# Performance work log

Measured on AMD Instinct MI355X. Metric: run time of the kernel, lower is better.

## Reference

```python
import jax, jax.numpy as jnp
import numpy as np
import math

B, N0, DEG = 32, 1584, 4
E = B * N0 * DEG
FIN, HID, EDIM, ROUTE, HEADS = 32, 64, 8, 16, 4
NEG = 0.2  # leaky_relu negative slope (alpha)
K1 = math.ceil(0.8 * N0)   # 1268 nodes/graph after pool1
K2 = math.ceil(0.8 * K1)   # 1015 after pool2
K3 = math.ceil(0.8 * K2)   # 812 after pool3


def _gatv2(x, src, dst, emask, edge_attr, Wl, bl, Wr, br, We, att, bo, num_nodes):
    # PyG GATv2Conv, concat=False (mean over heads), edge_dim, eval mode (no dropout)
    xl = (x @ Wl + bl).reshape(-1, HEADS, HID)            # source transform  [N,H,C]
    xr = (x @ Wr + br).reshape(-1, HEADS, HID)            # target transform  [N,H,C]
    ee = (edge_attr @ We).reshape(-1, HEADS, HID)         # edge transform    [E,H,C]
    m = jax.nn.leaky_relu(xl[src] + xr[dst] + ee, NEG)    # [E,H,C]
    logits = jnp.einsum('ehc,hc->eh', m, att)             # [E,H]
    logits = jnp.where(emask[:, None], logits, -jnp.inf)
    mx = jax.ops.segment_max(logits, dst, num_segments=num_nodes)
    mx = jnp.where(jnp.isfinite(mx), mx, 0.0)             # nodes w/o in-edges
    ex = jnp.where(emask[:, None], jnp.exp(logits - mx[dst]), 0.0)
    den = jax.ops.segment_sum(ex, dst, num_segments=num_nodes)
    alpha = ex / jnp.maximum(den[dst], 1e-16)             # segment softmax over dst
    out = jax.ops.segment_sum(alpha[:, :, None] * xl[src], dst, num_segments=num_nodes)
    return out.mean(axis=1) + bo                          # concat=False -> head mean


def _topk(x, src, dst, emask, w, n_per, k):
    # PyG TopKPooling(ratio=0.8): score = tanh(x.w/||w||); keep top-k per graph,
    # scale kept features by score; keep edges whose endpoints both survive.
    s = jnp.tanh((x @ w) / jnp.linalg.norm(w))            # [B*n_per]
    _, idx = jax.lax.top_k(s.reshape(B, n_per), k)        # [B,k]
    perm = (idx + jnp.arange(B)[:, None] * n_per).reshape(-1)
    x_new = x[perm] * s[perm][:, None]
    new_id = jnp.full((B * n_per,), -1, jnp.int32).at[perm].set(
        jnp.arange(B * k, dtype=jnp.int32))
    nsrc, ndst = new_id[src], new_id[dst]
    m = emask & (nsrc >= 0) & (ndst >= 0)
    return x_new, jnp.where(m, nsrc, 0), jnp.where(m, ndst, 0), m


def _readout(x, k):
    # global mean pool || global max pool (nodes are grouped per graph, k each)
    xb = x.reshape(B, k, HID)
    return jnp.concatenate([xb.mean(1), xb.max(1)], axis=1)


def _forward(x, edge_attr, edge_index,
             g1_Wl, g1_bl, g1_Wr, g1_br, g1_We, g1_att, g1_b,
             g2_Wl, g2_bl, g2_Wr, g2_br, g2_We, g2_att, g2_b,
             g3_Wl, g3_bl, g3_Wr, g3_br, g3_We, g3_att, g3_b,
             p1_w, p2_w, p3_w,
             fc1_W, fc1_b, fc2_W, fc2_b, fc3_W, fc3_b):
    src, dst = edge_index[0], edge_index[1]
    emask = jnp.ones((E,), bool)
    h = jax.nn.relu(_gatv2(x, src, dst, emask, edge_attr,
                           g1_Wl, g1_bl, g1_Wr, g1_br, g1_We, g1_att, g1_b, B * N0))
    h, src, dst, emask = _topk(h, src, dst, emask, p1_w, N0, K1)
    x1 = _readout(h, K1)
    h = jax.nn.relu(_gatv2(h, src, dst, emask, edge_attr,
                           g2_Wl, g2_bl, g2_Wr, g2_br, g2_We, g2_att, g2_b, B * K1))
    h, src, dst, emask = _topk(h, src, dst, emask, p2_w, K1, K2)
    x2 = _readout(h, K2)
    h = jax.nn.relu(_gatv2(h, src, dst, emask, edge_attr,
                           g3_Wl, g3_bl, g3_Wr, g3_br, g3_We, g3_att, g3_b, B * K2))
    h, src, dst, emask = _topk(h, src, dst, emask, p3_w, K2, K3)
    x3 = _readout(h, K3)
    r = x1 + x2 + x3                                      # [B, 2*HID]
    h = jax.nn.relu(r @ fc1_W + fc1_b)
    h = jax.nn.relu(h @ fc2_W + fc2_b)                    # dropout results unused in source
    return jax.nn.softmax(h @ fc3_W + fc3_b, axis=1)      # [B, ROUTE]


def setup_inputs() -> dict:
    key = jax.random.key(0)
    ks = iter(jax.random.split(key, 64))
    def nrm(shape, scale):
        return jax.random.normal(next(ks), shape, jnp.float32) * scale
    x = nrm((B * N0, FIN), 1.0)
    srcl = jax.random.randint(next(ks), (B, N0 * DEG), 0, N0)
    dstl = jax.random.randint(next(ks), (B, N0 * DEG), 0, N0)
    off = (jnp.arange(B) * N0)[:, None]
    edge_index = jnp.stack([(srcl + off).reshape(-1),
                            (dstl + off).reshape(-1)]).astype(jnp.int32)
    edge_attr = nrm((E, EDIM), 1.0)
    batch = jnp.repeat(jnp.arange(B, dtype=jnp.int32), N0)
    inp = {"x": x, "edge_attr": edge_attr, "edge_index": edge_index, "batch": batch}
    for li, fin in ((1, FIN), (2, HID), (3, HID)):
        g = 1.0 / np.sqrt(fin)
        inp[f"g{li}_Wl"] = nrm((fin, HEADS * HID), g)
        inp[f"g{li}_bl"] = nrm((HEADS * HID,), 0.02)
        inp[f"g{li}_Wr"] = nrm((fin, HEADS * HID), g)
        inp[f"g{li}_br"] = nrm((HEADS * HID,), 0.02)
        inp[f"g{li}_We"] = nrm((EDIM, HEADS * HID), 1.0 / np.sqrt(EDIM))
        inp[f"g{li}_att"] = nrm((HEADS, HID), 1.0 / np.sqrt(HID))
        inp[f"g{li}_b"] = nrm((HID,), 0.02)
    for li in (1, 2, 3):
        inp[f"p{li}_w"] = nrm((HID,), 1.0 / np.sqrt(HID))
    for fin, fout, nm in ((2 * HID, HID, "fc1"), (HID, HID, "fc2"), (HID, ROUTE, "fc3")):
        inp[f"{nm}_W"] = nrm((fin, fout), 1.0 / np.sqrt(fin))
        inp[f"{nm}_b"] = nrm((fout,), 0.02)
    return inp


def reference(x, edge_attr, edge_index, batch,
              g1_Wl, g1_bl, g1_Wr, g1_br, g1_We, g1_att, g1_b,
              g2_Wl, g2_bl, g2_Wr, g2_br, g2_We, g2_att, g2_b,
              g3_Wl, g3_bl, g3_Wr, g3_br, g3_We, g3_att, g3_b,
              p1_w, p2_w, p3_w,
              fc1_W, fc1_b, fc2_W, fc2_b, fc3_W, fc3_b):
    # batch is implicit: nodes are laid out grouped per graph with static sizes
    del batch
    return _forward(x, edge_attr, edge_index,
                    g1_Wl, g1_bl, g1_Wr, g1_br, g1_We, g1_att, g1_b,
                    g2_Wl, g2_bl, g2_Wr, g2_br, g2_We, g2_att, g2_b,
                    g3_Wl, g3_bl, g3_Wr, g3_br, g3_We, g3_att, g3_b,
                    p1_w, p2_w, p3_w,
                    fc1_W, fc1_b, fc2_W, fc2_b, fc3_W, fc3_b)
```

## Files before the change

kernel.cpp:

```cpp
#include <hip/hip_runtime.h>

typedef unsigned short u16;
typedef unsigned int u32;
typedef unsigned long long u64;

#define E_TOT 202752
#define NMAX  50688
#define HEADS 4
#define B_    32
#define MAXDEG 32

#define CDIV(a,b) (((a)+(b)-1)/(b))

__device__ __forceinline__ u32 ford(float f) {
  u32 u = __float_as_uint(f);
  return (u & 0x80000000u) ? ~u : (u | 0x80000000u);
}
__device__ __forceinline__ float ford_inv(u32 u) {
  u32 b = (u & 0x80000000u) ? (u ^ 0x80000000u) : ~u;
  return __uint_as_float(b);
}

__global__ void k_edge_init_csr(const int* __restrict__ ei, int* __restrict__ src,
                                int* __restrict__ dst, int* __restrict__ em,
                                int* __restrict__ cnt, int* __restrict__ csr) {
  int e = blockIdx.x * blockDim.x + threadIdx.x;
  if (e >= E_TOT) return;
  int s = ei[e], d = ei[E_TOT + e];
  src[e] = s;
  dst[e] = d;
  em[e] = 1;
  int pos = atomicAdd(&cnt[d], 1);
  if (pos < MAXDEG) csr[d * MAXDEG + pos] = e;
}

template <int FIN>
__global__ void k_transform_t(const float* __restrict__ hin,
                              const float* __restrict__ Wl, const float* __restrict__ bl,
                              const float* __restrict__ Wr, const float* __restrict__ br,
                              float* __restrict__ xl, float* __restrict__ xr) {
  __shared__ float xs[8][FIN];
  int n0 = blockIdx.x * 8, j = threadIdx.x;
  for (int t = j; t < 8 * FIN; t += 256)
    xs[t >> (FIN == 32 ? 5 : 6)][t & (FIN - 1)] =
        hin[(size_t)(n0 + (t >> (FIN == 32 ? 5 : 6))) * FIN + (t & (FIN - 1))];
  __syncthreads();
  float al[8], ar[8];
  float blv = bl[j], brv = br[j];
#pragma unroll
  for (int t = 0; t < 8; ++t) { al[t] = blv; ar[t] = brv; }
  for (int i = 0; i < FIN; ++i) {
    float wl = Wl[i * 256 + j], wr = Wr[i * 256 + j];
#pragma unroll
    for (int t = 0; t < 8; ++t) {
      float xv = xs[t][i];
      al[t] += xv * wl;
      ar[t] += xv * wr;
    }
  }
#pragma unroll
  for (int t = 0; t < 8; ++t) {
    xl[(size_t)(n0 + t) * 256 + j] = al[t];
    xr[(size_t)(n0 + t) * 256 + j] = ar[t];
  }
}

__global__ void k_gat_fused(const int* __restrict__ srcv, const int* __restrict__ cnt,
                            const int* __restrict__ csr, const float* __restrict__ ea,
                            const float* __restrict__ We, const float* __restrict__ att,
                            const float* __restrict__ xl, const float* __restrict__ xr,
                            const float* __restrict__ bias, const float* __restrict__ pwv,
                            float* __restrict__ out, float* __restrict__ sc, int N) {
  int n = blockIdx.x * 4 + (threadIdx.x >> 6);
  int lane = threadIdx.x & 63;
  int cg = lane & 15;
  int cb = (lane >> 4) * 64 + cg * 4;
  if (n >= N) return;
  int deg = min(cnt[n], MAXDEG);
  int e_l = 0, s_l = 0;
  if (lane < deg) { e_l = csr[n * MAXDEG + lane]; s_l = srcv[e_l]; }
  float4 xd4 = *(const float4*)(xr + (size_t)n * 256 + cb);
  float4 at4 = *(const float4*)(att + cb);
  float4 w0 = *(const float4*)(We + 0 * 256 + cb);
  float4 w1 = *(const float4*)(We + 1 * 256 + cb);
  float4 w2 = *(const float4*)(We + 2 * 256 + cb);
  float4 w3 = *(const float4*)(We + 3 * 256 + cb);
  float4 w4_ = *(const float4*)(We + 4 * 256 + cb);
  float4 w5 = *(const float4*)(We + 5 * 256 + cb);
  float4 w6 = *(const float4*)(We + 6 * 256 + cb);
  float4 w7 = *(const float4*)(We + 7 * 256 + cb);
  float m = -INFINITY, l = 0.f;
  float ox = 0.f, oy = 0.f, oz = 0.f, ow = 0.f;
  for (int i0 = 0; i0 < deg; i0 += 4) {
    int c0 = deg - i0; if (c0 > 4) c0 = 4;
    float4 xs[4], a0[4], a1[4];
#pragma unroll
    for (int j = 0; j < 4; ++j) {
      int idx = (j < c0) ? (i0 + j) : i0;
      int e = __shfl(e_l, idx, 64);
      int s = __shfl(s_l, idx, 64);
      xs[j] = *(const float4*)(xl + (size_t)s * 256 + cb);
      a0[j] = *(const float4*)(ea + (size_t)e * 8);
      a1[j] = *(const float4*)(ea + (size_t)e * 8 + 4);
    }
#pragma unroll
    for (int j = 0; j < 4; ++j) {
      if (j < c0) {
        float e0 = a0[j].x * w0.x + a0[j].y * w1.x + a0[j].z * w2.x + a0[j].w * w3.x
                 + a1[j].x * w4_.x + a1[j].y * w5.x + a1[j].z * w6.x + a1[j].w * w7.x;
        float e1 = a0[j].x * w0.y + a0[j].y * w1.y + a0[j].z * w2.y + a0[j].w * w3.y
                 + a1[j].x * w4_.y + a1[j].y * w5.y + a1[j].z * w6.y + a1[j].w * w7.y;
        float e2 = a0[j].x * w0.z + a0[j].y * w1.z + a0[j].z * w2.z + a0[j].w * w3.z
                 + a1[j].x * w4_.z + a1[j].y * w5.z + a1[j].z * w6.z + a1[j].w * w7.z;
        float e3 = a0[j].x * w0.w + a0[j].y * w1.w + a0[j].z * w2.w + a0[j].w * w3.w
                 + a1[j].x * w4_.w + a1[j].y * w5.w + a1[j].z * w6.w + a1[j].w * w7.w;
        float m0 = xs[j].x + xd4.x + e0; m0 = (m0 >= 0.f) ? m0 : 0.2f * m0;
        float m1 = xs[j].y + xd4.y + e1; m1 = (m1 >= 0.f) ? m1 : 0.2f * m1;
        float m2 = xs[j].z + xd4.z + e2; m2 = (m2 >= 0.f) ? m2 : 0.2f * m2;
        float m3 = xs[j].w + xd4.w + e3; m3 = (m3 >= 0.f) ? m3 : 0.2f * m3;
        float v = at4.x * m0 + at4.y * m1 + at4.z * m2 + at4.w * m3;
        v += __shfl_xor(v, 1, 64);
        v += __shfl_xor(v, 2, 64);
        v += __shfl_xor(v, 4, 64);
        v += __shfl_xor(v, 8, 64);
        float nm = fmaxf(m, v);
        float scale = __expf(m - nm);
        float p = __expf(v - nm);
        ox = ox * scale + p * xs[j].x;
        oy = oy * scale + p * xs[j].y;
        oz = oz * scale + p * xs[j].z;
        ow = ow * scale + p * xs[j].w;
        l = l * scale + p;
        m = nm;
      }
    }
  }
  float inv = 0.25f / fmaxf(l, 1e-16f);
  float r0 = ox * inv, r1 = oy * inv, r2 = oz * inv, r3 = ow * inv;
  r0 += __shfl_xor(r0, 16, 64); r0 += __shfl_xor(r0, 32, 64);
  r1 += __shfl_xor(r1, 16, 64); r1 += __shfl_xor(r1, 32, 64);
  r2 += __shfl_xor(r2, 16, 64); r2 += __shfl_xor(r2, 32, 64);
  r3 += __shfl_xor(r3, 16, 64); r3 += __shfl_xor(r3, 32, 64);
  float4 bi4 = *(const float4*)(bias + cg * 4);
  r0 = fmaxf(r0 + bi4.x, 0.f); r1 = fmaxf(r1 + bi4.y, 0.f);
  r2 = fmaxf(r2 + bi4.z, 0.f); r3 = fmaxf(r3 + bi4.w, 0.f);
  if (lane < 16) *(float4*)(out + (size_t)n * 64 + cg * 4) = float4{r0, r1, r2, r3};
  float4 pw4 = *(const float4*)(pwv + cg * 4);
  float dot = r0 * pw4.x + r1 * pw4.y + r2 * pw4.z + r3 * pw4.w;
  float wn = pw4.x * pw4.x + pw4.y * pw4.y + pw4.z * pw4.z + pw4.w * pw4.w;
  dot += __shfl_xor(dot, 1, 64); wn += __shfl_xor(wn, 1, 64);
  dot += __shfl_xor(dot, 2, 64); wn += __shfl_xor(wn, 2, 64);
  dot += __shfl_xor(dot, 4, 64); wn += __shfl_xor(wn, 4, 64);
  dot += __shfl_xor(dot, 8, 64); wn += __shfl_xor(wn, 8, 64);
  if (lane == 0) sc[n] = tanhf(dot / sqrtf(wn));
}

__global__ __launch_bounds__(1024) void k_topk(const float* __restrict__ s, int n_per,
                                               int k, int npad,
                                               int* __restrict__ perm, int* __restrict__ new_id) {
  __shared__ u64 kv[2048];
  int b = blockIdx.x, tid = threadIdx.x;
  int base = b * n_per;
  for (int i = tid; i < n_per; i += 1024) new_id[base + i] = -1;
  for (int i = tid; i < npad; i += 1024) {
    u32 sk = (i < n_per) ? ford(s[base + i]) : 0u;
    kv[i] = ((u64)sk << 32) | (u32)(0xFFFFFFFFu - (u32)i);
  }
  __syncthreads();
  for (int kk = 2; kk <= npad; kk <<= 1) {
    for (int j = kk >> 1; j > 0; j >>= 1) {
      for (int i = tid; i < npad; i += 1024) {
        int ixj = i ^ j;
        if (ixj > i) {
          u64 a = kv[i], c = kv[ixj];
          bool after = a < c;
          bool doswap = ((i & kk) == 0) ? after : !after;
          if (doswap) { kv[i] = c; kv[ixj] = a; }
        }
      }
      __syncthreads();
    }
  }
  for (int r = tid; r < k; r += 1024) {
    int old = (int)(0xFFFFFFFFu - (u32)(kv[r] & 0xFFFFFFFFu));
    perm[b * k + r] = base + old;
    new_id[base + old] = b * k + r;
  }
}

__global__ void k_gather(const float* __restrict__ hin, const float* __restrict__ s,
                         const int* __restrict__ perm, float* __restrict__ hout, int n64) {
  int t = blockIdx.x * blockDim.x + threadIdx.x;
  if (t >= n64) return;
  int i = t >> 6, c = t & 63;
  int g = perm[i];
  hout[t] = hin[(size_t)g * 64 + c] * s[g];
}

__global__ void k_remap_csr(int* __restrict__ src, int* __restrict__ dst,
                            int* __restrict__ em, const int* __restrict__ new_id,
                            int* __restrict__ cnt, int* __restrict__ csr) {
  int e = blockIdx.x * blockDim.x + threadIdx.x;
  if (e >= E_TOT) return;
  int ns = new_id[src[e]], nd = new_id[dst[e]];
  int m = em[e] && ns >= 0 && nd >= 0;
  src[e] = m ? ns : 0;
  dst[e] = m ? nd : 0;
  em[e] = m;
  if (m) {
    int pos = atomicAdd(&cnt[nd], 1);
    if (pos < MAXDEG) csr[nd * MAXDEG + pos] = e;
  }
}

__global__ void k_readout_part(const float* __restrict__ h, int k,
                               float* __restrict__ rsum, u32* __restrict__ rmaxI) {
  __shared__ float ps[256], pm[256];
  int b = blockIdx.x, ch = blockIdx.y, t = threadIdx.x;
  int c = t & 63, rg = t >> 6;
  int rpc = (k + 15) >> 4;
  int start = ch * rpc, end = min(k, start + rpc);
  const float* hb = h + (size_t)b * k * 64;
  float sum = 0.f, mx = -INFINITY;
  for (int i = start + rg; i < end; i += 4) {
    float v = hb[(size_t)i * 64 + c];
    sum += v;
    mx = fmaxf(mx, v);
  }
  ps[t] = sum; pm[t] = mx;
  __syncthreads();
  if (t < 64) {
    float s4 = ps[t] + ps[t + 64] + ps[t + 128] + ps[t + 192];
    float m4 = fmaxf(fmaxf(pm[t], pm[t + 64]), fmaxf(pm[t + 128], pm[t + 192]));
    atomicAdd(&rsum[b * 64 + t], s4);
    atomicMax(&rmaxI[b * 64 + t], ford(m4));
  }
}

__global__ void k_readout_fin(const float* __restrict__ rsum, const u32* __restrict__ rmaxI,
                              int k, float* __restrict__ r) {
  int b = blockIdx.x, c = threadIdx.x;
  if (c < 64) r[b * 128 + c] += rsum[b * 64 + c] / (float)k;
  else        r[b * 128 + c] += ford_inv(rmaxI[b * 64 + (c - 64)]);
}

__global__ void k_mlp(const float* __restrict__ r,
                      const float* __restrict__ W1, const float* __restrict__ b1,
                      const float* __restrict__ W2, const float* __restrict__ b2,
                      const float* __restrict__ W3, const float* __restrict__ b3,
                      float* __restrict__ out) {
  __shared__ float v0[128], v1[64], v2[64], lgts[16];
  int b = blockIdx.x, t = threadIdx.x;
  v0[t] = r[b * 128 + t];
  v0[64 + t] = r[b * 128 + 64 + t];
  __syncthreads();
  float a = b1[t];
  for (int i = 0; i < 128; ++i) a += v0[i] * W1[i * 64 + t];
  v1[t] = fmaxf(a, 0.f);
  __syncthreads();
  a = b2[t];
  for (int i = 0; i < 64; ++i) a += v1[i] * W2[i * 64 + t];
  v2[t] = fmaxf(a, 0.f);
  __syncthreads();
  if (t < 16) {
    a = b3[t];
    for (int i = 0; i < 64; ++i) a += v2[i] * W3[i * 16 + t];
    lgts[t] = a;
  }
  __syncthreads();
  if (t == 0) {
    float m = lgts[0];
    for (int j = 1; j < 16; ++j) m = fmaxf(m, lgts[j]);
    float ex[16], sum = 0.f;
    for (int j = 0; j < 16; ++j) { ex[j] = expf(lgts[j] - m); sum += ex[j]; }
    for (int j = 0; j < 16; ++j) out[b * 16 + j] = ex[j] / sum;
  }
}

extern "C" void kernel_launch(void* const* d_in, const int* in_sizes, int n_in,
                              void* d_out, int out_size, void* d_ws, size_t ws_size,
                              hipStream_t stream) {
  (void)in_sizes; (void)n_in; (void)out_size; (void)ws_size;
  const float* x  = (const float*)d_in[0];
  const float* ea = (const float*)d_in[1];
  const int*   ei = (const int*)d_in[2];

  const float *gWl[3], *gbl[3], *gWr[3], *gbr[3], *gWe[3], *gatt[3], *gb[3], *pw[3];
  for (int l = 0; l < 3; ++l) {
    int p0 = 4 + 7 * l;
    gWl[l]  = (const float*)d_in[p0 + 0];
    gbl[l]  = (const float*)d_in[p0 + 1];
    gWr[l]  = (const float*)d_in[p0 + 2];
    gbr[l]  = (const float*)d_in[p0 + 3];
    gWe[l]  = (const float*)d_in[p0 + 4];
    gatt[l] = (const float*)d_in[p0 + 5];
    gb[l]   = (const float*)d_in[p0 + 6];
    pw[l]   = (const float*)d_in[25 + l];
  }
  const float* fc1W = (const float*)d_in[28];
  const float* fc1b = (const float*)d_in[29];
  const float* fc2W = (const float*)d_in[30];
  const float* fc2b = (const float*)d_in[31];
  const float* fc3W = (const float*)d_in[32];
  const float* fc3b = (const float*)d_in[33];

  char* w = (char*)d_ws;
  size_t off = 0;
  auto alloc = [&](size_t bytes) -> void* {
    void* p = w + off;
    off += (bytes + 255) & ~(size_t)255;
    return p;
  };
  float* hbuf = (float*)alloc((size_t)B_ * 1268 * 64 * 4);
  float* xl   = (float*)alloc((size_t)NMAX * 256 * 4);
  float* xr   = (float*)alloc((size_t)NMAX * 256 * 4);
  float* nacc = (float*)alloc((size_t)NMAX * 64 * 4);
  int*   cnt  = (int*)alloc((size_t)NMAX * 4);
  char*  rblk = (char*)alloc(32 * 128 * 4);
  float* rsum = (float*)rblk;
  u32*   rmaxI= (u32*)(rblk + 32 * 64 * 4);
  int*   csr  = (int*)alloc((size_t)NMAX * MAXDEG * 4);
  float* sbuf = (float*)alloc((size_t)NMAX * 4);
  float* rbuf = (float*)alloc(32 * 128 * 4);
  int* src    = (int*)alloc((size_t)E_TOT * 4);
  int* dst    = (int*)alloc((size_t)E_TOT * 4);
  int* em     = (int*)alloc((size_t)E_TOT * 4);
  int* new_id = (int*)alloc((size_t)NMAX * 4);
  int* perm   = (int*)alloc((size_t)32 * 1268 * 4);

  hipMemsetAsync(cnt, 0, (size_t)NMAX * 4, stream);
  k_edge_init_csr<<<CDIV(E_TOT, 256), 256, 0, stream>>>(ei, src, dst, em, cnt, csr);
  hipMemsetAsync(rbuf, 0, 32 * 128 * 4, stream);

  const int Ns[3]    = {50688, 40576, 32480};
  const int npers[3] = {1584, 1268, 1015};
  const int ks[3]    = {1268, 1015, 812};
  const int npads[3] = {2048, 2048, 1024};

  for (int l = 0; l < 3; ++l) {
    int N = Ns[l];
    const float* hin = (l == 0) ? x : hbuf;
    hipMemsetAsync(rblk, 0, 32 * 128 * 4, stream);
    if (l == 0)
      k_transform_t<32><<<N / 8, 256, 0, stream>>>(hin, gWl[l], gbl[l], gWr[l], gbr[l], xl, xr);
    else
      k_transform_t<64><<<N / 8, 256, 0, stream>>>(hin, gWl[l], gbl[l], gWr[l], gbr[l], xl, xr);
    k_gat_fused<<<N / 4, 256, 0, stream>>>(src, cnt, csr, ea, gWe[l], gatt[l],
                                           xl, xr, gb[l], pw[l], nacc, sbuf, N);
    k_topk<<<32, 1024, 0, stream>>>(sbuf, npers[l], ks[l], npads[l], perm, new_id);
    k_gather<<<CDIV(B_ * ks[l] * 64, 256), 256, 0, stream>>>(nacc, sbuf, perm, hbuf,
                                                             B_ * ks[l] * 64);
    if (l < 2) {
      hipMemsetAsync(cnt, 0, (size_t)NMAX * 4, stream);
      k_remap_csr<<<CDIV(E_TOT, 256), 256, 0, stream>>>(src, dst, em, new_id, cnt, csr);
    }
    k_readout_part<<<dim3(32, 16), 256, 0, stream>>>(hbuf, ks[l], rsum, rmaxI);
    k_readout_fin<<<32, 128, 0, stream>>>(rsum, rmaxI, ks[l], rbuf);
  }
  k_mlp<<<32, 64, 0, stream>>>(rbuf, fc1W, fc1b, fc2W, fc2b, fc3W, fc3b, (float*)d_out);
}
```

Baseline: 562.4 us.

## Remap GAT blocks so each graph stays on one XCD and batch softmax updates

The fused GAT kernel now maps block indices so all blocks of a given graph land on the same XCD, given round-robin dispatch of blocks across the 8 XCDs. This keeps the xl/xr gathers for that graph in one XCD's L2 instead of spreading them over all of them. The edge loop is also restructured so four edges' logits are computed and reduced together, followed by one online-softmax rescale per group of four instead of per edge. A launch_bounds hint is added as well. The XCD mapping depends on the dispatch order and adds index arithmetic, and padding each graph to a multiple of 4 nodes adds a few idle waves.

```diff
diff --git a/kernel.cpp b/kernel.cpp
--- a/kernel.cpp
+++ b/kernel.cpp
@@ -65,17 +65,23 @@
   }
 }
 
-__global__ void k_gat_fused(const int* __restrict__ srcv, const int* __restrict__ cnt,
-                            const int* __restrict__ csr, const float* __restrict__ ea,
-                            const float* __restrict__ We, const float* __restrict__ att,
-                            const float* __restrict__ xl, const float* __restrict__ xr,
-                            const float* __restrict__ bias, const float* __restrict__ pwv,
-                            float* __restrict__ out, float* __restrict__ sc, int N) {
-  int n = blockIdx.x * 4 + (threadIdx.x >> 6);
+__global__ __launch_bounds__(256, 4)
+void k_gat_fused(const int* __restrict__ srcv, const int* __restrict__ cnt,
+                 const int* __restrict__ csr, const float* __restrict__ ea,
+                 const float* __restrict__ We, const float* __restrict__ att,
+                 const float* __restrict__ xl, const float* __restrict__ xr,
+                 const float* __restrict__ bias, const float* __restrict__ pwv,
+                 float* __restrict__ out, float* __restrict__ sc,
+                 int nper, int NB) {
+  int b = blockIdx.x;
+  int xcd = b & 7, slot = b >> 3;
+  int g = xcd + 8 * (slot / NB);
+  int ln = (slot % NB) * 4 + (threadIdx.x >> 6);
+  if (ln >= nper) return;
+  int n = g * nper + ln;
   int lane = threadIdx.x & 63;
   int cg = lane & 15;
   int cb = (lane >> 4) * 64 + cg * 4;
-  if (n >= N) return;
   int deg = min(cnt[n], MAXDEG);
   int e_l = 0, s_l = 0;
   if (lane < deg) { e_l = csr[n * MAXDEG + lane]; s_l = srcv[e_l]; }
@@ -93,47 +99,53 @@
   float ox = 0.f, oy = 0.f, oz = 0.f, ow = 0.f;
   for (int i0 = 0; i0 < deg; i0 += 4) {
     int c0 = deg - i0; if (c0 > 4) c0 = 4;
-    float4 xs[4], a0[4], a1[4];
+    float4 xs[4];
+    float v[4];
 #pragma unroll
     for (int j = 0; j < 4; ++j) {
       int idx = (j < c0) ? (i0 + j) : i0;
       int e = __shfl(e_l, idx, 64);
       int s = __shfl(s_l, idx, 64);
       xs[j] = *(const float4*)(xl + (size_t)s * 256 + cb);
-      a0[j] = *(const float4*)(ea + (size_t)e * 8);
-      a1[j] = *(const float4*)(ea + (size_t)e * 8 + 4);
-    }
-#pragma unroll
-    for (int j = 0; j < 4; ++j) {
-      if (j < c0) {
-        float e0 = a0[j].x * w0.x + a0[j].y * w1.x + a0[j].z * w2.x + a0[j].w * w3.x
-                 + a1[j].x * w4_.x + a1[j].y * w5.x + a1[j].z * w6.x + a1[j].w * w7.x;
-        float e1 = a0[j].x * w0.y + a0[j].y * w1.y + a0[j].z * w2.y + a0[j].w * w3.y
-                 + a1[j].x * w4_.y + a1[j].y * w5.y + a1[j].z * w6.y + a1[j].w * w7.y;
-        float e2 = a0[j].x * w0.z + a0[j].y * w1.z + a0[j].z * w2.z + a0[j].w * w3.z
-                 + a1[j].x * w4_.z + a1[j].y * w5.z + a1[j].z * w6.z + a1[j].w * w7.z;
-        float e3 = a0[j].x * w0.w + a0[j].y * w1.w + a0[j].z * w2.w + a0[j].w * w3.w
-                 + a1[j].x * w4_.w + a1[j].y * w5.w + a1[j].z * w6.w + a1[j].w * w7.w;
-        float m0 = xs[j].x + xd4.x + e0; m0 = (m0 >= 0.f) ? m0 : 0.2f * m0;
-        float m1 = xs[j].y + xd4.y + e1; m1 = (m1 >= 0.f) ? m1 : 0.2f * m1;
-        float m2 = xs[j].z + xd4.z + e2; m2 = (m2 >= 0.f) ? m2 : 0.2f * m2;
-        float m3 = xs[j].w + xd4.w + e3; m3 = (m3 >= 0.f) ? m3 : 0.2f * m3;
-        float v = at4.x * m0 + at4.y * m1 + at4.z * m2 + at4.w * m3;
-        v += __shfl_xor(v, 1, 64);
-        v += __shfl_xor(v, 2, 64);
-        v += __shfl_xor(v, 4, 64);
-        v += __shfl_xor(v, 8, 64);
-        float nm = fmaxf(m, v);
-        float scale = __expf(m - nm);
-        float p = __expf(v - nm);
-        ox = ox * scale + p * xs[j].x;
-        oy = oy * scale + p * xs[j].y;
-        oz = oz * scale + p * xs[j].z;
-        ow = ow * scale + p * xs[j].w;
-        l = l * scale + p;
-        m = nm;
-      }
-    }
+      float4 q0 = *(const float4*)(ea + (size_t)e * 8);
+      float4 q1 = *(const float4*)(ea + (size_t)e * 8 + 4);
+      float e0 = q0.x * w0.x + q0.y * w1.x + q0.z * w2.x + q0.w * w3.x
+               + q1.x * w4_.x + q1.y * w5.x + q1.z * w6.x + q1.w * w7.x;
+      float e1 = q0.x * w0.y + q0.y * w1.y + q0.z * w2.y + q0.w * w3.y
+               + q1.x * w4_.y + q1.y * w5.y + q1.z * w6.y + q1.w * w7.y;
+      float e2 = q0.x * w0.z + q0.y * w1.z + q0.z * w2.z + q0.w * w3.z
+               + q1.x * w4_.z + q1.y * w5.z + q1.z * w6.z + q1.w * w7.z;
+      float e3 = q0.x * w0.w + q0.y * w1.w + q0.z * w2.w + q0.w * w3.w
+               + q1.x * w4_.w + q1.y * w5.w + q1.z * w6.w + q1.w * w7.w;
+      float m0 = xs[j].x + xd4.x + e0; m0 = (m0 >= 0.f) ? m0 : 0.2f * m0;
+      float m1 = xs[j].y + xd4.y + e1; m1 = (m1 >= 0.f) ? m1 : 0.2f * m1;
+      float m2 = xs[j].z + xd4.z + e2; m2 = (m2 >= 0.f) ? m2 : 0.2f * m2;
+      float m3 = xs[j].w + xd4.w + e3; m3 = (m3 >= 0.f) ? m3 : 0.2f * m3;
+      v[j] = at4.x * m0 + at4.y * m1 + at4.z * m2 + at4.w * m3;
+    }
+#pragma unroll
+    for (int st = 1; st <= 8; st <<= 1) {
+      v[0] += __shfl_xor(v[0], st, 64);
+      v[1] += __shfl_xor(v[1], st, 64);
+      v[2] += __shfl_xor(v[2], st, 64);
+      v[3] += __shfl_xor(v[3], st, 64);
+    }
+    float vmax = v[0];
+    if (c0 > 1) vmax = fmaxf(vmax, v[1]);
+    if (c0 > 2) vmax = fmaxf(vmax, v[2]);
+    if (c0 > 3) vmax = fmaxf(vmax, v[3]);
+    float nm = fmaxf(m, vmax);
+    float scale = __expf(m - nm);
+    float p0 = __expf(v[0] - nm);
+    float p1 = (c0 > 1) ? __expf(v[1] - nm) : 0.f;
+    float p2 = (c0 > 2) ? __expf(v[2] - nm) : 0.f;
+    float p3 = (c0 > 3) ? __expf(v[3] - nm) : 0.f;
+    ox = ox * scale + p0 * xs[0].x + p1 * xs[1].x + p2 * xs[2].x + p3 * xs[3].x;
+    oy = oy * scale + p0 * xs[0].y + p1 * xs[1].y + p2 * xs[2].y + p3 * xs[3].y;
+    oz = oz * scale + p0 * xs[0].z + p1 * xs[1].z + p2 * xs[2].z + p3 * xs[3].z;
+    ow = ow * scale + p0 * xs[0].w + p1 * xs[1].w + p2 * xs[2].w + p3 * xs[3].w;
+    l = l * scale + p0 + p1 + p2 + p3;
+    m = nm;
   }
   float inv = 0.25f / fmaxf(l, 1e-16f);
   float r0 = ox * inv, r1 = oy * inv, r2 = oz * inv, r3 = ow * inv;
@@ -339,15 +351,17 @@
 
   for (int l = 0; l < 3; ++l) {
     int N = Ns[l];
+    int nper = npers[l];
+    int NBg = CDIV(nper, 4);
     const float* hin = (l == 0) ? x : hbuf;
     hipMemsetAsync(rblk, 0, 32 * 128 * 4, stream);
     if (l == 0)
       k_transform_t<32><<<N / 8, 256, 0, stream>>>(hin, gWl[l], gbl[l], gWr[l], gbr[l], xl, xr);
     else
       k_transform_t<64><<<N / 8, 256, 0, stream>>>(hin, gWl[l], gbl[l], gWr[l], gbr[l], xl, xr);
-    k_gat_fused<<<N / 4, 256, 0, stream>>>(src, cnt, csr, ea, gWe[l], gatt[l],
-                                           xl, xr, gb[l], pw[l], nacc, sbuf, N);
-    k_topk<<<32, 1024, 0, stream>>>(sbuf, npers[l], ks[l], npads[l], perm, new_id);
+    k_gat_fused<<<32 * NBg, 256, 0, stream>>>(src, cnt, csr, ea, gWe[l], gatt[l],
+                                              xl, xr, gb[l], pw[l], nacc, sbuf, nper, NBg);
+    k_topk<<<32, 1024, 0, stream>>>(sbuf, nper, ks[l], npads[l], perm, new_id);
     k_gather<<<CDIV(B_ * ks[l] * 64, 256), 256, 0, stream>>>(nacc, sbuf, perm, hbuf,
                                                              B_ * ks[l] * 64);
     if (l < 2) {
```

Measured after the change: 614.8 us. +9.3%, slower.

## Map GAT blocks to graphs per XCD and process four nodes per wavefront

Applied to the files above, without the earlier changes.

The GAT aggregation kernel now assigns each block a graph chosen by an XCD-aware swizzle. The aim is to keep a graph's source features (xl) in the same XCD's L2, since edges stay within a graph. Each wavefront handles four consecutive nodes and prefetches the next node's CSR, degree and xr before computing the current one, amortising the We/att/bias loads and the weight-norm reduction. This lowers block count and parallelism, adds per-node register pressure (launch bounds 256,4), and assumes blocks are dispatched round-robin across 8 XCDs.

```diff
diff --git a/kernel.cpp b/kernel.cpp
--- a/kernel.cpp
+++ b/kernel.cpp
@@ -65,21 +65,22 @@
   }
 }
 
-__global__ void k_gat_fused(const int* __restrict__ srcv, const int* __restrict__ cnt,
-                            const int* __restrict__ csr, const float* __restrict__ ea,
-                            const float* __restrict__ We, const float* __restrict__ att,
-                            const float* __restrict__ xl, const float* __restrict__ xr,
-                            const float* __restrict__ bias, const float* __restrict__ pwv,
-                            float* __restrict__ out, float* __restrict__ sc, int N) {
-  int n = blockIdx.x * 4 + (threadIdx.x >> 6);
+__global__ __launch_bounds__(256, 4)
+void k_gat_fused(const int* __restrict__ srcv, const int* __restrict__ cnt,
+                 const int* __restrict__ csr, const float* __restrict__ ea,
+                 const float* __restrict__ We, const float* __restrict__ att,
+                 const float* __restrict__ xl, const float* __restrict__ xr,
+                 const float* __restrict__ bias, const float* __restrict__ pwv,
+                 float* __restrict__ out, float* __restrict__ sc,
+                 int nper, int NB) {
+  int b = blockIdx.x;
+  int xcd = b & 7, slot = b >> 3;
+  int g = xcd + 8 * (slot / NB);
+  int ln0 = (slot % NB) * 16 + (threadIdx.x >> 6) * 4;
   int lane = threadIdx.x & 63;
   int cg = lane & 15;
   int cb = (lane >> 4) * 64 + cg * 4;
-  if (n >= N) return;
-  int deg = min(cnt[n], MAXDEG);
-  int e_l = 0, s_l = 0;
-  if (lane < deg) { e_l = csr[n * MAXDEG + lane]; s_l = srcv[e_l]; }
-  float4 xd4 = *(const float4*)(xr + (size_t)n * 256 + cb);
+  int nbase = g * nper;
   float4 at4 = *(const float4*)(att + cb);
   float4 w0 = *(const float4*)(We + 0 * 256 + cb);
   float4 w1 = *(const float4*)(We + 1 * 256 + cb);
@@ -89,70 +90,103 @@
   float4 w5 = *(const float4*)(We + 5 * 256 + cb);
   float4 w6 = *(const float4*)(We + 6 * 256 + cb);
   float4 w7 = *(const float4*)(We + 7 * 256 + cb);
-  float m = -INFINITY, l = 0.f;
-  float ox = 0.f, oy = 0.f, oz = 0.f, ow = 0.f;
-  for (int i0 = 0; i0 < deg; i0 += 4) {
-    int c0 = deg - i0; if (c0 > 4) c0 = 4;
-    float4 xs[4], a0[4], a1[4];
-#pragma unroll
-    for (int j = 0; j < 4; ++j) {
-      int idx = (j < c0) ? (i0 + j) : i0;
-      int e = __shfl(e_l, idx, 64);
-      int s = __shfl(s_l, idx, 64);
-      xs[j] = *(const float4*)(xl + (size_t)s * 256 + cb);
-      a0[j] = *(const float4*)(ea + (size_t)e * 8);
-      a1[j] = *(const float4*)(ea + (size_t)e * 8 + 4);
-    }
-#pragma unroll
-    for (int j = 0; j < 4; ++j) {
-      if (j < c0) {
-        float e0 = a0[j].x * w0.x + a0[j].y * w1.x + a0[j].z * w2.x + a0[j].w * w3.x
-                 + a1[j].x * w4_.x + a1[j].y * w5.x + a1[j].z * w6.x + a1[j].w * w7.x;
-        float e1 = a0[j].x * w0.y + a0[j].y * w1.y + a0[j].z * w2.y + a0[j].w * w3.y
-                 + a1[j].x * w4_.y + a1[j].y * w5.y + a1[j].z * w6.y + a1[j].w * w7.y;
-        float e2 = a0[j].x * w0.z + a0[j].y * w1.z + a0[j].z * w2.z + a0[j].w * w3.z
-                 + a1[j].x * w4_.z + a1[j].y * w5.z + a1[j].z * w6.z + a1[j].w * w7.z;
-        float e3 = a0[j].x * w0.w + a0[j].y * w1.w + a0[j].z * w2.w + a0[j].w * w3.w
-                 + a1[j].x * w4_.w + a1[j].y * w5.w + a1[j].z * w6.w + a1[j].w * w7.w;
-        float m0 = xs[j].x + xd4.x + e0; m0 = (m0 >= 0.f) ? m0 : 0.2f * m0;
-        float m1 = xs[j].y + xd4.y + e1; m1 = (m1 >= 0.f) ? m1 : 0.2f * m1;
-        float m2 = xs[j].z + xd4.z + e2; m2 = (m2 >= 0.f) ? m2 : 0.2f * m2;
-        float m3 = xs[j].w + xd4.w + e3; m3 = (m3 >= 0.f) ? m3 : 0.2f * m3;
-        float v = at4.x * m0 + at4.y * m1 + at4.z * m2 + at4.w * m3;
-        v += __shfl_xor(v, 1, 64);
-        v += __shfl_xor(v, 2, 64);
-        v += __shfl_xor(v, 4, 64);
-        v += __shfl_xor(v, 8, 64);
-        float nm = fmaxf(m, v);
-        float scale = __expf(m - nm);
-        float p = __expf(v - nm);
-        ox = ox * scale + p * xs[j].x;
-        oy = oy * scale + p * xs[j].y;
-        oz = oz * scale + p * xs[j].z;
-        ow = ow * scale + p * xs[j].w;
-        l = l * scale + p;
-        m = nm;
+  float4 bi4 = *(const float4*)(bias + cg * 4);
+  float4 pw4 = *(const float4*)(pwv + cg * 4);
+  float wn = pw4.x * pw4.x + pw4.y * pw4.y + pw4.z * pw4.z + pw4.w * pw4.w;
+  wn += __shfl_xor(wn, 1, 64); wn += __shfl_xor(wn, 2, 64);
+  wn += __shfl_xor(wn, 4, 64); wn += __shfl_xor(wn, 8, 64);
+  float isq = 1.f / sqrtf(wn);
+
+  int ln = ln0;
+  bool valid = ln < nper;
+  int n = nbase + ln;
+  int deg = 0, e_l = 0, s_l = 0;
+  float4 xd4 = float4{0.f, 0.f, 0.f, 0.f};
+  if (valid) {
+    deg = min(cnt[n], MAXDEG);
+    if (lane < deg) { e_l = csr[n * MAXDEG + lane]; s_l = srcv[e_l]; }
+    xd4 = *(const float4*)(xr + (size_t)n * 256 + cb);
+  }
+
+  for (int i = 0; i < 4; ++i) {
+    bool cval = valid; int curn = n, cdeg = deg, ce = e_l, cs = s_l;
+    float4 cxd = xd4;
+    if (i < 3) {
+      ln = ln0 + i + 1;
+      valid = ln < nper;
+      n = nbase + ln;
+      deg = 0; e_l = 0; s_l = 0;
+      xd4 = float4{0.f, 0.f, 0.f, 0.f};
+      if (valid) {
+        deg = min(cnt[n], MAXDEG);
+        if (lane < deg) { e_l = csr[n * MAXDEG + lane]; s_l = srcv[e_l]; }
+        xd4 = *(const float4*)(xr + (size_t)n * 256 + cb);
       }
     }
-  }
-  float inv = 0.25f / fmaxf(l, 1e-16f);
-  float r0 = ox * inv, r1 = oy * inv, r2 = oz * inv, r3 = ow * inv;
-  r0 += __shfl_xor(r0, 16, 64); r0 += __shfl_xor(r0, 32, 64);
-  r1 += __shfl_xor(r1, 16, 64); r1 += __shfl_xor(r1, 32, 64);
-  r2 += __shfl_xor(r2, 16, 64); r2 += __shfl_xor(r2, 32, 64);
-  r3 += __shfl_xor(r3, 16, 64); r3 += __shfl_xor(r3, 32, 64);
-  float4 bi4 = *(const float4*)(bias + cg * 4);
-  r0 = fmaxf(r0 + bi4.x, 0.f); r1 = fmaxf(r1 + bi4.y, 0.f);
-  r2 = fmaxf(r2 + bi4.z, 0.f); r3 = fmaxf(r3 + bi4.w, 0.f);
-  if (lane < 16) *(float4*)(out + (size_t)n * 64 + cg * 4) = float4{r0, r1, r2, r3};
-  float4 pw4 = *(const float4*)(pwv + cg * 4);
-  float dot = r0 * pw4.x + r1 * pw4.y + r2 * pw4.z + r3 * pw4.w;
-  float wn = pw4.x * pw4.x + pw4.y * pw4.y + pw4.z * pw4.z + pw4.w * pw4.w;
-  dot += __shfl_xor(dot, 1, 64); wn += __shfl_xor(wn, 1, 64);
-  dot += __shfl_xor(dot, 2, 64); wn += __shfl_xor(wn, 2, 64);
-  dot += __shfl_xor(dot, 4, 64); wn += __shfl_xor(wn, 4, 64);
-  dot += __shfl_xor(dot, 8, 64); wn += __shfl_xor(wn, 8, 64);
-  if (lane == 0) sc[n] = tanhf(dot / sqrtf(wn));
+    if (!cval) continue;
+
+    float m = -INFINITY, l = 0.f;
+    float ox = 0.f, oy = 0.f, oz = 0.f, ow = 0.f;
+    for (int i0 = 0; i0 < cdeg; i0 += 4) {
+      int c0 = cdeg - i0; if (c0 > 4) c0 = 4;
+      float4 xs[4], a0[4], a1[4];
+#pragma unroll
+      for (int j = 0; j < 4; ++j) {
+        int idx = (j < c0) ? (i0 + j) : i0;
+        int e = __shfl(ce, idx, 64);
+        int s = __shfl(cs, idx, 64);
+        xs[j] = *(const float4*)(xl + (size_t)s * 256 + cb);
+        a0[j] = *(const float4*)(ea + (size_t)e * 8);
+        a1[j] = *(const float4*)(ea + (size_t)e * 8 + 4);
+      }
+#pragma unroll
+      for (int j = 0; j < 4; ++j) {
+        if (j < c0) {
+          float e0 = a0[j].x * w0.x + a0[j].y * w1.x + a0[j].z * w2.x + a0[j].w * w3.x
+                   + a1[j].x * w4_.x + a1[j].y * w5.x + a1[j].z * w6.x + a1[j].w * w7.x;
+          float e1 = a0[j].x * w0.y + a0[j].y * w1.y + a0[j].z * w2.y + a0[j].w * w3.y
+                   + a1[j].x * w4_.y + a1[j].y * w5.y + a1[j].z * w6.y + a1[j].w * w7.y;
+          float e2 = a0[j].x * w0.z + a0[j].y * w1.z + a0[j].z * w2.z + a0[j].w * w3.z
+                   + a1[j].x * w4_.z + a1[j].y * w5.z + a1[j].z * w6.z + a1[j].w * w7.z;
+          float e3 = a0[j].x * w0.w + a0[j].y * w1.w + a0[j].z * w2.w + a0[j].w * w3.w
+                   + a1[j].x * w4_.w + a1[j].y * w5.w + a1[j].z * w6.w + a1[j].w * w7.w;
+          float m0 = xs[j].x + cxd.x + e0; m0 = (m0 >= 0.f) ? m0 : 0.2f * m0;
+          float m1 = xs[j].y + cxd.y + e1; m1 = (m1 >= 0.f) ? m1 : 0.2f * m1;
+          float m2 = xs[j].z + cxd.z + e2; m2 = (m2 >= 0.f) ? m2 : 0.2f * m2;
+          float m3 = xs[j].w + cxd.w + e3; m3 = (m3 >= 0.f) ? m3 : 0.2f * m3;
+          float v = at4.x * m0 + at4.y * m1 + at4.z * m2 + at4.w * m3;
+          v += __shfl_xor(v, 1, 64);
+          v += __shfl_xor(v, 2, 64);
+          v += __shfl_xor(v, 4, 64);
+          v += __shfl_xor(v, 8, 64);
+          float nm = fmaxf(m, v);
+          float scale = __expf(m - nm);
+          float p = __expf(v - nm);
+          ox = ox * scale + p * xs[j].x;
+          oy = oy * scale + p * xs[j].y;
+          oz = oz * scale + p * xs[j].z;
+          ow = ow * scale + p * xs[j].w;
+          l = l * scale + p;
+          m = nm;
+        }
+      }
+    }
+    float inv = 0.25f / fmaxf(l, 1e-16f);
+    float r0 = ox * inv, r1 = oy * inv, r2 = oz * inv, r3 = ow * inv;
+    r0 += __shfl_xor(r0, 16, 64); r0 += __shfl_xor(r0, 32, 64);
+    r1 += __shfl_xor(r1, 16, 64); r1 += __shfl_xor(r1, 32, 64);
+    r2 += __shfl_xor(r2, 16, 64); r2 += __shfl_xor(r2, 32, 64);
+    r3 += __shfl_xor(r3, 16, 64); r3 += __shfl_xor(r3, 32, 64);
+    r0 = fmaxf(r0 + bi4.x, 0.f); r1 = fmaxf(r1 + bi4.y, 0.f);
+    r2 = fmaxf(r2 + bi4.z, 0.f); r3 = fmaxf(r3 + bi4.w, 0.f);
+    if (lane < 16) *(float4*)(out + (size_t)curn * 64 + cg * 4) = float4{r0, r1, r2, r3};
+    float dot = r0 * pw4.x + r1 * pw4.y + r2 * pw4.z + r3 * pw4.w;
+    dot += __shfl_xor(dot, 1, 64);
+    dot += __shfl_xor(dot, 2, 64);
+    dot += __shfl_xor(dot, 4, 64);
+    dot += __shfl_xor(dot, 8, 64);
+    if (lane == 0) sc[curn] = tanhf(dot * isq);
+  }
 }
 
 __global__ __launch_bounds__(1024) void k_topk(const float* __restrict__ s, int n_per,
@@ -339,15 +373,17 @@
 
   for (int l = 0; l < 3; ++l) {
     int N = Ns[l];
+    int nper = npers[l];
+    int NBg = CDIV(nper, 16);
     const float* hin = (l == 0) ? x : hbuf;
     hipMemsetAsync(rblk, 0, 32 * 128 * 4, stream);
     if (l == 0)
       k_transform_t<32><<<N / 8, 256, 0, stream>>>(hin, gWl[l], gbl[l], gWr[l], gbr[l], xl, xr);
     else
       k_transform_t<64><<<N / 8, 256, 0, stream>>>(hin, gWl[l], gbl[l], gWr[l], gbr[l], xl, xr);
-    k_gat_fused<<<N / 4, 256, 0, stream>>>(src, cnt, csr, ea, gWe[l], gatt[l],
-                                           xl, xr, gb[l], pw[l], nacc, sbuf, N);
-    k_topk<<<32, 1024, 0, stream>>>(sbuf, npers[l], ks[l], npads[l], perm, new_id);
+    k_gat_fused<<<32 * NBg, 256, 0, stream>>>(src, cnt, csr, ea, gWe[l], gatt[l],
+                                              xl, xr, gb[l], pw[l], nacc, sbuf, nper, NBg);
+    k_topk<<<32, 1024, 0, stream>>>(sbuf, nper, ks[l], npads[l], perm, new_id);
     k_gather<<<CDIV(B_ * ks[l] * 64, 256), 256, 0, stream>>>(nacc, sbuf, perm, hbuf,
                                                              B_ * ks[l] * 64);
     if (l < 2) {
```

Measured after the change: 595.4 us. +5.9%, slower.

## Fuse top-k gather with readout and widen node tile in transform kernel

Applied to the files above, without the earlier changes.

The gather kernel now also computes per-graph sum/max partials with atomics, removing the separate readout pass that re-read the pooled features. Readout accumulators get one slot per layer, zeroed once up front, which drops the per-layer memset. The transform kernel processes 16 nodes per block with a transposed shared tile read as float4, halving weight loads per node. The pool-weight norm is computed before the edge loop instead of at the end. Risks: many more atomics (one block per 4 nodes) and higher register use from 32 accumulators.

```diff
diff --git a/kernel.cpp b/kernel.cpp
--- a/kernel.cpp
+++ b/kernel.cpp
@@ -39,27 +39,42 @@
                               const float* __restrict__ Wl, const float* __restrict__ bl,
                               const float* __restrict__ Wr, const float* __restrict__ br,
                               float* __restrict__ xl, float* __restrict__ xr) {
-  __shared__ float xs[8][FIN];
-  int n0 = blockIdx.x * 8, j = threadIdx.x;
-  for (int t = j; t < 8 * FIN; t += 256)
-    xs[t >> (FIN == 32 ? 5 : 6)][t & (FIN - 1)] =
-        hin[(size_t)(n0 + (t >> (FIN == 32 ? 5 : 6))) * FIN + (t & (FIN - 1))];
-  __syncthreads();
-  float al[8], ar[8];
+  __shared__ float xs[FIN][20];
+  int n0 = blockIdx.x * 16, j = threadIdx.x;
+  for (int t = j; t < 16 * FIN; t += 256) {
+    int nd = t >> (FIN == 32 ? 5 : 6), f = t & (FIN - 1);
+    xs[f][nd] = hin[(size_t)(n0 + nd) * FIN + f];
+  }
+  __syncthreads();
+  float al[16], ar[16];
   float blv = bl[j], brv = br[j];
 #pragma unroll
-  for (int t = 0; t < 8; ++t) { al[t] = blv; ar[t] = brv; }
+  for (int t = 0; t < 16; ++t) { al[t] = blv; ar[t] = brv; }
   for (int i = 0; i < FIN; ++i) {
     float wl = Wl[i * 256 + j], wr = Wr[i * 256 + j];
+    float4 x0 = *(const float4*)&xs[i][0];
+    float4 x1 = *(const float4*)&xs[i][4];
+    float4 x2 = *(const float4*)&xs[i][8];
+    float4 x3 = *(const float4*)&xs[i][12];
+    al[0]  += x0.x * wl; ar[0]  += x0.x * wr;
+    al[1]  += x0.y * wl; ar[1]  += x0.y * wr;
+    al[2]  += x0.z * wl; ar[2]  += x0.z * wr;
+    al[3]  += x0.w * wl; ar[3]  += x0.w * wr;
+    al[4]  += x1.x * wl; ar[4]  += x1.x * wr;
+    al[5]  += x1.y * wl; ar[5]  += x1.y * wr;
+    al[6]  += x1.z * wl; ar[6]  += x1.z * wr;
+    al[7]  += x1.w * wl; ar[7]  += x1.w * wr;
+    al[8]  += x2.x * wl; ar[8]  += x2.x * wr;
+    al[9]  += x2.y * wl; ar[9]  += x2.y * wr;
+    al[10] += x2.z * wl; ar[10] += x2.z * wr;
+    al[11] += x2.w * wl; ar[11] += x2.w * wr;
+    al[12] += x3.x * wl; ar[12] += x3.x * wr;
+    al[13] += x3.y * wl; ar[13] += x3.y * wr;
+    al[14] += x3.z * wl; ar[14] += x3.z * wr;
+    al[15] += x3.w * wl; ar[15] += x3.w * wr;
+  }
 #pragma unroll
-    for (int t = 0; t < 8; ++t) {
-      float xv = xs[t][i];
-      al[t] += xv * wl;
-      ar[t] += xv * wr;
-    }
-  }
-#pragma unroll
-  for (int t = 0; t < 8; ++t) {
+  for (int t = 0; t < 16; ++t) {
     xl[(size_t)(n0 + t) * 256 + j] = al[t];
     xr[(size_t)(n0 + t) * 256 + j] = ar[t];
   }
@@ -89,6 +104,11 @@
   float4 w5 = *(const float4*)(We + 5 * 256 + cb);
   float4 w6 = *(const float4*)(We + 6 * 256 + cb);
   float4 w7 = *(const float4*)(We + 7 * 256 + cb);
+  float4 pw4 = *(const float4*)(pwv + cg * 4);
+  float wn = pw4.x * pw4.x + pw4.y * pw4.y + pw4.z * pw4.z + pw4.w * pw4.w;
+  wn += __shfl_xor(wn, 1, 64); wn += __shfl_xor(wn, 2, 64);
+  wn += __shfl_xor(wn, 4, 64); wn += __shfl_xor(wn, 8, 64);
+  float isq = 1.f / sqrtf(wn);
   float m = -INFINITY, l = 0.f;
   float ox = 0.f, oy = 0.f, oz = 0.f, ow = 0.f;
   for (int i0 = 0; i0 < deg; i0 += 4) {
@@ -145,14 +165,12 @@
   r0 = fmaxf(r0 + bi4.x, 0.f); r1 = fmaxf(r1 + bi4.y, 0.f);
   r2 = fmaxf(r2 + bi4.z, 0.f); r3 = fmaxf(r3 + bi4.w, 0.f);
   if (lane < 16) *(float4*)(out + (size_t)n * 64 + cg * 4) = float4{r0, r1, r2, r3};
-  float4 pw4 = *(const float4*)(pwv + cg * 4);
   float dot = r0 * pw4.x + r1 * pw4.y + r2 * pw4.z + r3 * pw4.w;
-  float wn = pw4.x * pw4.x + pw4.y * pw4.y + pw4.z * pw4.z + pw4.w * pw4.w;
-  dot += __shfl_xor(dot, 1, 64); wn += __shfl_xor(wn, 1, 64);
-  dot += __shfl_xor(dot, 2, 64); wn += __shfl_xor(wn, 2, 64);
-  dot += __shfl_xor(dot, 4, 64); wn += __shfl_xor(wn, 4, 64);
-  dot += __shfl_xor(dot, 8, 64); wn += __shfl_xor(wn, 8, 64);
-  if (lane == 0) sc[n] = tanhf(dot / sqrtf(wn));
+  dot += __shfl_xor(dot, 1, 64);
+  dot += __shfl_xor(dot, 2, 64);
+  dot += __shfl_xor(dot, 4, 64);
+  dot += __shfl_xor(dot, 8, 64);
+  if (lane == 0) sc[n] = tanhf(dot * isq);
 }
 
 __global__ __launch_bounds__(1024) void k_topk(const float* __restrict__ s, int n_per,
@@ -188,13 +206,29 @@
   }
 }
 
-__global__ void k_gather(const float* __restrict__ hin, const float* __restrict__ s,
-                         const int* __restrict__ perm, float* __restrict__ hout, int n64) {
-  int t = blockIdx.x * blockDim.x + threadIdx.x;
-  if (t >= n64) return;
-  int i = t >> 6, c = t & 63;
-  int g = perm[i];
-  hout[t] = hin[(size_t)g * 64 + c] * s[g];
+__global__ void k_gather_ro(const float* __restrict__ hin, const float* __restrict__ s,
+                            const int* __restrict__ perm, float* __restrict__ hout,
+                            int k, float* __restrict__ rsum, u32* __restrict__ rmaxI) {
+  __shared__ float ps[256], pm[256];
+  int b = blockIdx.x, t = threadIdx.x;
+  int i = blockIdx.y * 4 + (t >> 6);
+  int c = t & 63;
+  bool valid = i < k;
+  float v = 0.f;
+  if (valid) {
+    int g = perm[b * k + i];
+    v = hin[(size_t)g * 64 + c] * s[g];
+    hout[((size_t)b * k + i) * 64 + c] = v;
+  }
+  ps[t] = valid ? v : 0.f;
+  pm[t] = valid ? v : -INFINITY;
+  __syncthreads();
+  if (t < 64) {
+    float s4 = ps[t] + ps[t + 64] + ps[t + 128] + ps[t + 192];
+    float m4 = fmaxf(fmaxf(pm[t], pm[t + 64]), fmaxf(pm[t + 128], pm[t + 192]));
+    atomicAdd(&rsum[b * 64 + t], s4);
+    atomicMax(&rmaxI[b * 64 + t], ford(m4));
+  }
 }
 
 __global__ void k_remap_csr(int* __restrict__ src, int* __restrict__ dst,
@@ -213,30 +247,6 @@
   }
 }
 
-__global__ void k_readout_part(const float* __restrict__ h, int k,
-                               float* __restrict__ rsum, u32* __restrict__ rmaxI) {
-  __shared__ float ps[256], pm[256];
-  int b = blockIdx.x, ch = blockIdx.y, t = threadIdx.x;
-  int c = t & 63, rg = t >> 6;
-  int rpc = (k + 15) >> 4;
-  int start = ch * rpc, end = min(k, start + rpc);
-  const float* hb = h + (size_t)b * k * 64;
-  float sum = 0.f, mx = -INFINITY;
-  for (int i = start + rg; i < end; i += 4) {
-    float v = hb[(size_t)i * 64 + c];
-    sum += v;
-    mx = fmaxf(mx, v);
-  }
-  ps[t] = sum; pm[t] = mx;
-  __syncthreads();
-  if (t < 64) {
-    float s4 = ps[t] + ps[t + 64] + ps[t + 128] + ps[t + 192];
-    float m4 = fmaxf(fmaxf(pm[t], pm[t + 64]), fmaxf(pm[t + 128], pm[t + 192]));
-    atomicAdd(&rsum[b * 64 + t], s4);
-    atomicMax(&rmaxI[b * 64 + t], ford(m4));
-  }
-}
-
 __global__ void k_readout_fin(const float* __restrict__ rsum, const u32* __restrict__ rmaxI,
                               int k, float* __restrict__ r) {
   int b = blockIdx.x, c = threadIdx.x;
@@ -316,9 +326,7 @@
   float* xr   = (float*)alloc((size_t)NMAX * 256 * 4);
   float* nacc = (float*)alloc((size_t)NMAX * 64 * 4);
   int*   cnt  = (int*)alloc((size_t)NMAX * 4);
-  char*  rblk = (char*)alloc(32 * 128 * 4);
-  float* rsum = (float*)rblk;
-  u32*   rmaxI= (u32*)(rblk + 32 * 64 * 4);
+  char*  rblk = (char*)alloc(3 * 32 * 128 * 4);
   int*   csr  = (int*)alloc((size_t)NMAX * MAXDEG * 4);
   float* sbuf = (float*)alloc((size_t)NMAX * 4);
   float* rbuf = (float*)alloc(32 * 128 * 4);
@@ -329,8 +337,9 @@
   int* perm   = (int*)alloc((size_t)32 * 1268 * 4);
 
   hipMemsetAsync(cnt, 0, (size_t)NMAX * 4, stream);
+  hipMemsetAsync(rblk, 0, 3 * 32 * 128 * 4, stream);
+  hipMemsetAsync(rbuf, 0, 32 * 128 * 4, stream);
   k_edge_init_csr<<<CDIV(E_TOT, 256), 256, 0, stream>>>(ei, src, dst, em, cnt, csr);
-  hipMemsetAsync(rbuf, 0, 32 * 128 * 4, stream);
 
   const int Ns[3]    = {50688, 40576, 32480};
   const int npers[3] = {1584, 1268, 1015};
@@ -340,21 +349,21 @@
   for (int l = 0; l < 3; ++l) {
     int N = Ns[l];
     const float* hin = (l == 0) ? x : hbuf;
-    hipMemsetAsync(rblk, 0, 32 * 128 * 4, stream);
+    float* rsum = (float*)(rblk + l * 32 * 128 * 4);
+    u32* rmaxI  = (u32*)(rblk + l * 32 * 128 * 4 + 32 * 64 * 4);
     if (l == 0)
-      k_transform_t<32><<<N / 8, 256, 0, stream>>>(hin, gWl[l], gbl[l], gWr[l], gbr[l], xl, xr);
+      k_transform_t<32><<<N / 16, 256, 0, stream>>>(hin, gWl[l], gbl[l], gWr[l], gbr[l], xl, xr);
     else
-      k_transform_t<64><<<N / 8, 256, 0, stream>>>(hin, gWl[l], gbl[l], gWr[l], gbr[l], xl, xr);
+      k_transform_t<64><<<N / 16, 256, 0, stream>>>(hin, gWl[l], gbl[l], gWr[l], gbr[l], xl, xr);
     k_gat_fused<<<N / 4, 256, 0, stream>>>(src, cnt, csr, ea, gWe[l], gatt[l],
                                            xl, xr, gb[l], pw[l], nacc, sbuf, N);
     k_topk<<<32, 1024, 0, stream>>>(sbuf, npers[l], ks[l], npads[l], perm, new_id);
-    k_gather<<<CDIV(B_ * ks[l] * 64, 256), 256, 0, stream>>>(nacc, sbuf, perm, hbuf,
-                                                             B_ * ks[l] * 64);
+    k_gather_ro<<<dim3(32, CDIV(ks[l], 4)), 256, 0, stream>>>(nacc, sbuf, perm, hbuf,
+                                                              ks[l], rsum, rmaxI);
     if (l < 2) {
       hipMemsetAsync(cnt, 0, (size_t)NMAX * 4, stream);
       k_remap_csr<<<CDIV(E_TOT, 256), 256, 0, stream>>>(src, dst, em, new_id, cnt, csr);
     }
-    k_readout_part<<<dim3(32, 16), 256, 0, stream>>>(hbuf, ks[l], rsum, rmaxI);
     k_readout_fin<<<32, 128, 0, stream>>>(rsum, rmaxI, ks[l], rbuf);
   }
   k_mlp<<<32, 64, 0, stream>>>(rbuf, fc1W, fc1b, fc2W, fc2b, fc3W, fc3b, (float*)d_out);
```

After: 550.2 us. -2.2%, faster.
